# Kernel optimization log

Hardware: AMD Instinct MI355X
Metric: run time of the kernel (lower is better)

## Reference

```python
import jax, jax.numpy as jnp
import numpy as np

N_HEADS = 16
N_EMBD = 1024

def setup_inputs() -> dict:
    key = jax.random.key(0)
    k1, k2, k3, k4, k5 = jax.random.split(key, 5)
    B, T, C = 4, 2048, N_EMBD
    x = jax.random.normal(k1, (B, T, C), dtype=jnp.float32)
    # Linear weights stored as [in, out] (equivalent math to torch's x @ W.T + b)
    W_attn = jax.random.normal(k2, (C, 3 * C), dtype=jnp.float32) * 0.02
    b_attn = jax.random.normal(k3, (3 * C,), dtype=jnp.float32) * 0.02
    W_proj = jax.random.normal(k4, (C, C), dtype=jnp.float32) * 0.02
    b_proj = jax.random.normal(k5, (C,), dtype=jnp.float32) * 0.02
    return {"x": x, "W_attn": W_attn, "b_attn": b_attn, "W_proj": W_proj, "b_proj": b_proj}

def reference(x, W_attn, b_attn, W_proj, b_proj):
    B, T, C = x.shape
    H = N_HEADS
    D = C // H
    scale = 1.0 / jnp.sqrt(jnp.asarray(D, dtype=x.dtype))
    # fused QKV projection
    qkv = x @ W_attn + b_attn                      # [B, T, 3C]
    q, k, v = jnp.split(qkv, 3, axis=-1)           # each [B, T, C]
    q = q.reshape(B, T, H, D)
    k = k.reshape(B, T, H, D)
    v = v.reshape(B, T, H, D)
    # non-causal SDPA
    scores = jnp.einsum('bqhd,bkhd->bhqk', q, k) * scale  # [B, H, T, T]
    attn = jax.nn.softmax(scores, axis=-1)
    y = jnp.einsum('bhqk,bkhd->bqhd', attn, v)     # [B, T, H, D]
    y = y.reshape(B, T, C)
    return y @ W_proj + b_proj
```

## Files before the change

kernel.cpp:

```cpp
#include <hip/hip_runtime.h>

typedef short s16x8 __attribute__((ext_vector_type(8)));
typedef short s16x4 __attribute__((ext_vector_type(4)));
typedef float f32x4 __attribute__((ext_vector_type(4)));

__device__ __forceinline__ unsigned short f2bf(float f) {
  unsigned u = __float_as_uint(f);
  u += 0x7fffu + ((u >> 16) & 1u);
  return (unsigned short)(u >> 16);
}
__device__ __forceinline__ float bf2f(unsigned short h) {
  return __uint_as_float(((unsigned)h) << 16);
}

#define GLOAD_LDS16(g, l)                                          \
  __builtin_amdgcn_global_load_lds(                                \
      (const __attribute__((address_space(1))) void*)(g),          \
      (__attribute__((address_space(3))) void*)(l), 16, 0, 0)


__global__ __launch_bounds__(256) void cvt_x_bf16(const float* __restrict__ in,
                                                  unsigned short* __restrict__ out) {
  int i = (blockIdx.x * 256 + threadIdx.x) * 4;
  float4 v = *(const float4*)(in + i);
  ushort4 o;
  o.x = f2bf(v.x); o.y = f2bf(v.y); o.z = f2bf(v.z); o.w = f2bf(v.w);
  *(ushort4*)(out + i) = o;
}

__global__ __launch_bounds__(256) void transpose_w(const float* __restrict__ W,
                                                   unsigned short* __restrict__ Wt,
                                                   int R, int C) {
  __shared__ float tile[32][33];
  int c0 = blockIdx.x * 32, r0 = blockIdx.y * 32;
  int x = threadIdx.x, ty = threadIdx.y;
  for (int yy = ty; yy < 32; yy += 8)
    tile[yy][x] = W[(size_t)(r0 + yy) * C + c0 + x];
  __syncthreads();
  for (int yy = ty; yy < 32; yy += 8)
    Wt[(size_t)(c0 + yy) * R + r0 + x] = f2bf(tile[x][yy]);
}

__global__ __launch_bounds__(256) void transpose_v(const unsigned short* __restrict__ qkv,
                                                   unsigned short* __restrict__ vt) {
  __shared__ unsigned short TT[32][72];
  const int bh = blockIdx.y;
  const int t0 = blockIdx.x * 32;
  const int b = bh >> 4, h = bh & 15;
  const int t = threadIdx.x;
  {
    int row = t >> 3, c8 = (t & 7) * 8;
    const unsigned short* src =
        qkv + (size_t)(b * 2048 + t0 + row) * 3072 + 2048 + h * 64 + c8;
    *(uint4*)&TT[row][c8] = *(const uint4*)src;
  }
  __syncthreads();
  {
    int drow = t >> 2, tc8 = (t & 3) * 8;
    uint4 val;
    unsigned short* vp = (unsigned short*)&val;
    for (int j = 0; j < 8; j++) vp[j] = TT[tc8 + j][drow];
    *(uint4*)(vt + (size_t)(bh * 64 + drow) * 2048 + t0 + tc8) = val;
  }
}


template <bool OUT_BF16>
__global__ __launch_bounds__(256) void gemm_bt(const unsigned short* __restrict__ A,
                                               const unsigned short* __restrict__ Bt,
                                               const float* __restrict__ bias,
                                               void* __restrict__ Cout,
                                               int M, int N, int K) {
  __shared__ __align__(16) unsigned short As[128 * 32];
  __shared__ __align__(16) unsigned short Bs[128 * 32];

  const int tid  = threadIdx.x;
  const int lane = tid & 63;
  const int w    = tid >> 6;
  const int lr   = lane & 15;
  const int quad = lane >> 4;
  const int wm   = (w >> 1) * 64;
  const int wn   = (w & 1) * 64;
  const int m0   = blockIdx.x * 128;
  const int n0   = blockIdx.y * 128;

  f32x4 acc[4][4];
  for (int i = 0; i < 4; i++)
    for (int j = 0; j < 4; j++)
      acc[i][j] = f32x4{0.f, 0.f, 0.f, 0.f};

  const int srow = tid >> 2;
  const int scb  = (tid & 3) * 8;
  const unsigned short* Ap = A  + (size_t)(m0 + srow) * K + scb;
  const unsigned short* Bp = Bt + (size_t)(n0 + srow) * K + scb;
  unsigned short* lA0 = As + w * 512;
  unsigned short* lA1 = As + 2048 + w * 512;
  unsigned short* lB0 = Bs + w * 512;
  unsigned short* lB1 = Bs + 2048 + w * 512;

  for (int kk = 0; kk < K; kk += 32) {
    __syncthreads();
    GLOAD_LDS16(Ap + kk, lA0);
    GLOAD_LDS16(Ap + (size_t)64 * K + kk, lA1);
    GLOAD_LDS16(Bp + kk, lB0);
    GLOAD_LDS16(Bp + (size_t)64 * K + kk, lB1);
    __syncthreads();

    s16x8 af[4], bf[4];
    for (int i = 0; i < 4; i++) af[i] = *(const s16x8*)&As[(wm + i * 16 + lr) * 32 + quad * 8];
    for (int j = 0; j < 4; j++) bf[j] = *(const s16x8*)&Bs[(wn + j * 16 + lr) * 32 + quad * 8];
    for (int i = 0; i < 4; i++)
      for (int j = 0; j < 4; j++)
        acc[i][j] = __builtin_amdgcn_mfma_f32_16x16x32_bf16(af[i], bf[j], acc[i][j], 0, 0, 0);
  }

  for (int j = 0; j < 4; j++) {
    int col = n0 + wn + j * 16 + lr;
    float bc = bias[col];
    for (int i = 0; i < 4; i++) {
      int rowb = m0 + wm + i * 16 + quad * 4;
      for (int r = 0; r < 4; r++) {
        float v = acc[i][j][r] + bc;
        if (OUT_BF16)
          ((unsigned short*)Cout)[(size_t)(rowb + r) * N + col] = f2bf(v);
        else
          ((float*)Cout)[(size_t)(rowb + r) * N + col] = v;
      }
    }
  }
}


__global__ __launch_bounds__(256, 4) void attn_flash(const unsigned short* __restrict__ qkv,
                                                     const unsigned short* __restrict__ vt,
                                                     unsigned short* __restrict__ y) {
  const int T = 2048, C3 = 3072;
  const int bh = blockIdx.x & 63;
  const int qt = blockIdx.x >> 6;
  const int b  = bh >> 4;
  const int h  = bh & 15;
  const int q0 = qt * 128;

  const int tid  = threadIdx.x;
  const int lane = tid & 63;
  const int w    = tid >> 6;
  const int lr   = lane & 15;
  const int quad = lane >> 4;

  __shared__ __align__(16) unsigned short Ks[64][64];
  __shared__ __align__(16) unsigned short Vs[64][64];

  s16x8 qf[2][2];
  const float QSC = 0.18033688f;
  for (int j = 0; j < 2; j++)
    for (int c = 0; c < 2; c++) {
      const unsigned short* qp =
          qkv + (size_t)(b * T + q0 + w * 32 + j * 16 + lr) * C3 + h * 64 + c * 32 + quad * 8;
      s16x8 t = *(const s16x8*)qp;
      s16x8 o;
      for (int e = 0; e < 8; e++)
        o[e] = (short)f2bf(bf2f((unsigned short)t[e]) * QSC);
      qf[j][c] = o;
    }

  s16x8 ones;
  for (int e = 0; e < 8; e++) ones[e] = (short)0x3F80;

  f32x4 O[2][4];
  f32x4 Lacc[2];
  for (int j = 0; j < 2; j++) {
    for (int dt = 0; dt < 4; dt++) O[j][dt] = f32x4{0.f, 0.f, 0.f, 0.f};
    Lacc[j] = f32x4{0.f, 0.f, 0.f, 0.f};
  }

  const int srow = tid >> 3;
  const int sc8  = (tid & 7) * 8;
  const int scb  = sc8 * 2;
  const unsigned short* kbase = qkv + (size_t)(b * T) * C3 + 1024 + (size_t)h * 64;
  const unsigned short* vbase = vt + (size_t)(bh * 64) * 2048;
  char* KsB = (char*)Ks;
  char* VsB = (char*)Vs;
  const int rswz = (lr & 7) << 4;

  for (int kt = 0; kt < 32; kt++) {
    const int k0 = kt * 64;
    __syncthreads();
    for (int rr = 0; rr < 64; rr += 32) {
      int row = srow + rr;
      int r32 = row & 31;
      int key = (row & ~31) | (((r32 & 12) << 1) | ((r32 >> 4) << 2) | (r32 & 3));
      int sw  = scb ^ ((row & 7) << 4);
      *(uint4*)(KsB + row * 128 + sw) =
          *(const uint4*)(kbase + (size_t)(k0 + key) * C3 + sc8);
      *(uint4*)(VsB + row * 128 + sw) =
          *(const uint4*)(vbase + (size_t)row * 2048 + k0 + sc8);
    }
    __syncthreads();

    for (int ch = 0; ch < 2; ch++) {
      const char* krowA = KsB + (ch * 32 + lr) * 128;
      const char* krowB = KsB + (ch * 32 + 16 + lr) * 128;
      s16x8 kA0 = *(const s16x8*)(krowA + ((quad * 16) ^ rswz));
      s16x8 kA1 = *(const s16x8*)(krowA + ((64 + quad * 16) ^ rswz));
      s16x8 kB0 = *(const s16x8*)(krowB + ((quad * 16) ^ rswz));
      s16x8 kB1 = *(const s16x8*)(krowB + ((64 + quad * 16) ^ rswz));
      s16x8 vf[4];
      for (int dt = 0; dt < 4; dt++)
        vf[dt] = *(const s16x8*)(VsB + (dt * 16 + lr) * 128 + ((ch * 64 + quad * 16) ^ rswz));

      for (int j = 0; j < 2; j++) {
        f32x4 Sa = f32x4{0.f, 0.f, 0.f, 0.f};
        f32x4 Sb = f32x4{0.f, 0.f, 0.f, 0.f};
        Sa = __builtin_amdgcn_mfma_f32_16x16x32_bf16(kA0, qf[j][0], Sa, 0, 0, 0);
        Sa = __builtin_amdgcn_mfma_f32_16x16x32_bf16(kA1, qf[j][1], Sa, 0, 0, 0);
        Sb = __builtin_amdgcn_mfma_f32_16x16x32_bf16(kB0, qf[j][0], Sb, 0, 0, 0);
        Sb = __builtin_amdgcn_mfma_f32_16x16x32_bf16(kB1, qf[j][1], Sb, 0, 0, 0);
        unsigned u0 = __float_as_uint(__builtin_amdgcn_exp2f(Sa[0])) + 0x8000u;
        unsigned u1 = __float_as_uint(__builtin_amdgcn_exp2f(Sa[1])) + 0x8000u;
        unsigned u2 = __float_as_uint(__builtin_amdgcn_exp2f(Sa[2])) + 0x8000u;
        unsigned u3 = __float_as_uint(__builtin_amdgcn_exp2f(Sa[3])) + 0x8000u;
        unsigned u4 = __float_as_uint(__builtin_amdgcn_exp2f(Sb[0])) + 0x8000u;
        unsigned u5 = __float_as_uint(__builtin_amdgcn_exp2f(Sb[1])) + 0x8000u;
        unsigned u6 = __float_as_uint(__builtin_amdgcn_exp2f(Sb[2])) + 0x8000u;
        unsigned u7 = __float_as_uint(__builtin_amdgcn_exp2f(Sb[3])) + 0x8000u;
        union { unsigned u[4]; s16x8 v; } pk;
        pk.u[0] = __builtin_amdgcn_perm(u1, u0, 0x07060302u);
        pk.u[1] = __builtin_amdgcn_perm(u3, u2, 0x07060302u);
        pk.u[2] = __builtin_amdgcn_perm(u5, u4, 0x07060302u);
        pk.u[3] = __builtin_amdgcn_perm(u7, u6, 0x07060302u);
        Lacc[j] = __builtin_amdgcn_mfma_f32_16x16x32_bf16(pk.v, ones, Lacc[j], 0, 0, 0);
        for (int dt = 0; dt < 4; dt++)
          O[j][dt] = __builtin_amdgcn_mfma_f32_16x16x32_bf16(pk.v, vf[dt], O[j][dt], 0, 0, 0);
      }
    }
  }

  for (int j = 0; j < 2; j++) {
    for (int r = 0; r < 4; r++) {
      float inv = 1.f / Lacc[j][r];
      int row = b * T + q0 + w * 32 + j * 16 + quad * 4 + r;
      for (int dt = 0; dt < 4; dt++) {
        int col = h * 64 + dt * 16 + lr;
        y[(size_t)row * 1024 + col] = f2bf(O[j][dt][r] * inv);
      }
    }
  }
}


extern "C" void kernel_launch(void* const* d_in, const int* in_sizes, int n_in,
                              void* d_out, int out_size, void* d_ws, size_t ws_size,
                              hipStream_t stream) {
  const float* x  = (const float*)d_in[0];
  const float* Wa = (const float*)d_in[1];
  const float* ba = (const float*)d_in[2];
  const float* Wp = (const float*)d_in[3];
  const float* bp = (const float*)d_in[4];
  float* out = (float*)d_out;

  char* ws = (char*)d_ws;
  unsigned short* xb  = (unsigned short*)ws;
  unsigned short* Wat = (unsigned short*)(ws + 16777216);
  unsigned short* Wpt = (unsigned short*)(ws + 23068672);
  unsigned short* qkv = (unsigned short*)(ws + 25165824);
  unsigned short* vtr = (unsigned short*)(ws + 75497472);

  cvt_x_bf16<<<8192, 256, 0, stream>>>(x, xb);
  transpose_w<<<dim3(96, 32), dim3(32, 8), 0, stream>>>(Wa, Wat, 1024, 3072);
  transpose_w<<<dim3(32, 32), dim3(32, 8), 0, stream>>>(Wp, Wpt, 1024, 1024);

  gemm_bt<true><<<dim3(64, 24), 256, 0, stream>>>(xb, Wat, ba, qkv, 8192, 3072, 1024);

  transpose_v<<<dim3(64, 64), 256, 0, stream>>>(qkv, vtr);

  attn_flash<<<1024, 256, 0, stream>>>(qkv, vtr, xb);

  gemm_bt<false><<<dim3(64, 8), 256, 0, stream>>>(xb, Wpt, bp, out, 8192, 1024, 1024);
}
```

Baseline: 283.9 us.

## Double-buffer K/V tiles with async global-to-LDS loads in flash attention

Replaces the synchronous register-staged K/V tile loads with `global_load_lds` DMA into a two-slot shared-memory ring. The next tile is prefetched while MFMAs run on the current one, and the per-iteration barriers drop from two to one. The XOR swizzle and the key-row permutation move from the LDS write address to the global source address, because the DMA writes each wave's lanes to contiguous LDS. LDS use doubles and correctness depends on the compiler waiting for the outstanding vector-memory loads before the barrier.

```diff
diff --git a/kernel.cpp b/kernel.cpp
--- a/kernel.cpp
+++ b/kernel.cpp
@@ -147,8 +147,8 @@
   const int lr   = lane & 15;
   const int quad = lane >> 4;
 
-  __shared__ __align__(16) unsigned short Ks[64][64];
-  __shared__ __align__(16) unsigned short Vs[64][64];
+  __shared__ __align__(16) unsigned short Ks[2][64][64];
+  __shared__ __align__(16) unsigned short Vs[2][64][64];
 
   s16x8 qf[2][2];
   const float QSC = 0.18033688f;
@@ -174,28 +174,34 @@
   }
 
   const int srow = tid >> 3;
-  const int sc8  = (tid & 7) * 8;
-  const int scb  = sc8 * 2;
+  const int scol = (((tid & 7) ^ (srow & 7)) * 8);
+  const int kperm = (((srow & 12) << 1) | ((srow >> 4) << 2) | (srow & 3));
+
   const unsigned short* kbase = qkv + (size_t)(b * T) * C3 + 1024 + (size_t)h * 64;
   const unsigned short* vbase = vt + (size_t)(bh * 64) * 2048;
-  char* KsB = (char*)Ks;
-  char* VsB = (char*)Vs;
+  const unsigned short* kp0 = kbase + (size_t)(kperm)      * C3 + scol;
+  const unsigned short* kp1 = kbase + (size_t)(32 + kperm) * C3 + scol;
+  const unsigned short* vp0 = vbase + (size_t)(srow)      * 2048 + scol;
+  const unsigned short* vp1 = vbase + (size_t)(srow + 32) * 2048 + scol;
+
+#define STAGE_KV(bb, k0off)                                                  \
+  do {                                                                       \
+    GLOAD_LDS16(kp0 + (size_t)(k0off) * C3, &Ks[bb][w * 8][0]);              \
+    GLOAD_LDS16(kp1 + (size_t)(k0off) * C3, &Ks[bb][w * 8 + 32][0]);         \
+    GLOAD_LDS16(vp0 + (k0off), &Vs[bb][w * 8][0]);                           \
+    GLOAD_LDS16(vp1 + (k0off), &Vs[bb][w * 8 + 32][0]);                      \
+  } while (0)
+
   const int rswz = (lr & 7) << 4;
 
+  STAGE_KV(0, 0);
+  int cur = 0;
   for (int kt = 0; kt < 32; kt++) {
-    const int k0 = kt * 64;
     __syncthreads();
-    for (int rr = 0; rr < 64; rr += 32) {
-      int row = srow + rr;
-      int r32 = row & 31;
-      int key = (row & ~31) | (((r32 & 12) << 1) | ((r32 >> 4) << 2) | (r32 & 3));
-      int sw  = scb ^ ((row & 7) << 4);
-      *(uint4*)(KsB + row * 128 + sw) =
-          *(const uint4*)(kbase + (size_t)(k0 + key) * C3 + sc8);
-      *(uint4*)(VsB + row * 128 + sw) =
-          *(const uint4*)(vbase + (size_t)row * 2048 + k0 + sc8);
-    }
-    __syncthreads();
+    if (kt < 31) STAGE_KV(cur ^ 1, (kt + 1) * 64);
+
+    const char* KsB = (const char*)&Ks[cur][0][0];
+    const char* VsB = (const char*)&Vs[cur][0][0];
 
     for (int ch = 0; ch < 2; ch++) {
       const char* krowA = KsB + (ch * 32 + lr) * 128;
@@ -233,7 +239,9 @@
           O[j][dt] = __builtin_amdgcn_mfma_f32_16x16x32_bf16(pk.v, vf[dt], O[j][dt], 0, 0, 0);
       }
     }
-  }
+    cur ^= 1;
+  }
+#undef STAGE_KV
 
   for (int j = 0; j < 2; j++) {
     for (int r = 0; r < 4; r++) {
```

Measured after the change: 280.1 us. No clear change (-1.4%).
